# Optimization experiments

Hardware: AMD Instinct MI355X
Metric: run time of the kernel (lower is better)

## Reference

```python
import jax, jax.numpy as jnp
import numpy as np
from jax import lax

D_MODEL = 1024
D_STATE = 16
D_CONV = 4
EXPAND = 2
D_INNER = D_MODEL * EXPAND
EPS = 1e-6


def setup_inputs() -> dict:
    key = jax.random.key(0)
    ks = jax.random.split(key, 8)
    B, L = 2, 1024
    x = jax.random.normal(ks[0], (B, L, D_MODEL), dtype=jnp.float32)
    norm_w = jnp.ones((D_MODEL,), jnp.float32)
    W_in = jax.random.normal(ks[1], (2 * D_INNER, D_MODEL), jnp.float32) * (1.0 / np.sqrt(D_MODEL))
    conv_w = jax.random.normal(ks[2], (D_INNER, 1, D_CONV), jnp.float32) * (1.0 / np.sqrt(D_CONV))
    conv_b = jnp.zeros((D_INNER,), jnp.float32)
    W_x = jax.random.normal(ks[3], (2 * D_STATE + 1, D_INNER), jnp.float32) * (1.0 / np.sqrt(D_INNER))
    A_log = jnp.log(jnp.broadcast_to(jnp.arange(1, D_STATE + 1, dtype=jnp.float32), (D_INNER, D_STATE)))
    D_skip = jnp.ones((D_INNER,), jnp.float32)
    W_dt = jax.random.normal(ks[4], (D_INNER, 1), jnp.float32)
    b_dt = jax.random.normal(ks[5], (D_INNER,), jnp.float32) * 0.1
    W_out = jax.random.normal(ks[6], (D_MODEL, D_INNER), jnp.float32) * (1.0 / np.sqrt(D_INNER))
    return {"x": x, "norm_w": norm_w, "W_in": W_in, "conv_w": conv_w, "conv_b": conv_b,
            "W_x": W_x, "A_log": A_log, "D_skip": D_skip, "W_dt": W_dt, "b_dt": b_dt, "W_out": W_out}


def _selective_scan(x, delta, A, Bp, Cp, D_skip):
    # x, delta: (B, L, D); A: (D, N); Bp, Cp: (B, L, N)
    Bb, L, Dd = x.shape
    N = A.shape[1]

    def step(h, t_in):
        delta_t, B_t, C_t, x_t = t_in           # (B,D),(B,N),(B,N),(B,D)
        dA = jnp.exp(delta_t[..., None] * A)    # (B,D,N)
        h = dA * h + (delta_t * x_t)[..., None] * B_t[:, None, :]
        y_t = jnp.einsum('bdn,bn->bd', h, C_t)
        return h, y_t

    xs = (jnp.moveaxis(delta, 1, 0), jnp.moveaxis(Bp, 1, 0),
          jnp.moveaxis(Cp, 1, 0), jnp.moveaxis(x, 1, 0))
    h0 = jnp.zeros((Bb, Dd, N), x.dtype)
    _, ys = lax.scan(step, h0, xs)              # ys: (L,B,D)
    return jnp.moveaxis(ys, 0, 1) + x * D_skip


def reference(x, norm_w, W_in, conv_w, conv_b, W_x, A_log, D_skip, W_dt, b_dt, W_out):
    residual = x
    # RMSNorm
    xn = x * lax.rsqrt(jnp.mean(x * x, axis=-1, keepdims=True) + EPS) * norm_w
    # in_proj and split
    xz = xn @ W_in.T                              # (B,L,2*Din)
    x_ssm, z = jnp.split(xz, 2, axis=-1)
    # causal depthwise conv1d
    xc = jnp.swapaxes(x_ssm, 1, 2)                # (B,Din,L)
    xc = lax.conv_general_dilated(xc, conv_w, window_strides=(1,),
                                  padding=[(D_CONV - 1, 0)],
                                  feature_group_count=D_INNER,
                                  dimension_numbers=('NCH', 'OIH', 'NCH'))
    xc = xc + conv_b[None, :, None]
    x_ssm = jax.nn.silu(jnp.swapaxes(xc, 1, 2))   # (B,L,Din)
    # input-dependent SSM params
    ssm_params = x_ssm @ W_x.T                    # (B,L,2N+1)
    B_param = ssm_params[:, :, :D_STATE]
    C_param = ssm_params[:, :, D_STATE:2 * D_STATE]
    dt_raw = ssm_params[:, :, -1:]                # (B,L,1)
    delta = jax.nn.softplus(dt_raw * W_dt[:, 0] + b_dt)  # (B,L,Din)
    A = -jnp.exp(A_log)
    y = _selective_scan(x_ssm, delta, A, B_param, C_param, D_skip)
    y = y * jax.nn.silu(z)
    y = y @ W_out.T
    return y + residual
```

## Files before the change

### kernel.cpp

```cpp
#include <hip/hip_runtime.h>
#include <math.h>

#define D_MODEL 1024
#define D_STATE 16
#define D_CONV  4
#define D_INNER 2048
#define LSEQ    1024
#define BATCH   2
#define NROWS   (BATCH * LSEQ)
#define EPSV    1e-6f

#define CHUNK   16
#define NCHUNK  (LSEQ / CHUNK)
#define SSTATE  (BATCH * D_INNER * D_STATE)
#define SROW    36

typedef __attribute__((ext_vector_type(8))) short bf16x8;
typedef __attribute__((ext_vector_type(4))) float f32x4;

__device__ __forceinline__ float silu_f(float x) { return x / (1.0f + __expf(-x)); }
__device__ __forceinline__ float softplus_f(float x) {
    return (x > 20.0f) ? x : __logf(1.0f + __expf(x));
}
__device__ __forceinline__ unsigned short f2bf(float f) {
    unsigned int u = __float_as_uint(f);
    unsigned int r = (u + 0x7FFFu + ((u >> 16) & 1u)) >> 16;
    return (unsigned short)r;
}

__device__ __forceinline__ void pow16(float e1, float* p) {
    float e2 = e1 * e1, e4 = e2 * e2, e8 = e4 * e4;
    p[0] = e1;       p[1] = e2;       p[2] = e2 * e1;  p[3] = e4;
    p[4] = e4 * e1;  p[5] = e4 * e2;  p[6] = e4 * p[2]; p[7] = e8;
    p[8] = e8 * e1;  p[9] = e8 * e2;  p[10] = e8 * p[2]; p[11] = e8 * e4;
    p[12] = e8 * p[4]; p[13] = e8 * p[5]; p[14] = e8 * p[6]; p[15] = e8 * e8;
}

#define WIN_F4   (2 * D_INNER * D_MODEL / 4)
#define WOUT_F4  (D_MODEL * D_INNER / 4)
#define CVT_BLKS ((WIN_F4 + WOUT_F4) / 256)
__global__ __launch_bounds__(256) void prep_kernel(const float* __restrict__ x,
                                                   const float* __restrict__ w,
                                                   unsigned short* __restrict__ xnb,
                                                   const float* __restrict__ w_in,
                                                   unsigned short* __restrict__ w_in_b,
                                                   const float* __restrict__ w_out,
                                                   unsigned short* __restrict__ w_out_b) {
    int blk = blockIdx.x;
    if (blk < NROWS) {
        int row = blk;
        const float4* xr = (const float4*)(x + (size_t)row * D_MODEL);
        float4 v = xr[threadIdx.x];
        float s = v.x * v.x + v.y * v.y + v.z * v.z + v.w * v.w;
#pragma unroll
        for (int off = 32; off > 0; off >>= 1) s += __shfl_down(s, off, 64);
        __shared__ float wsum[4];
        int lane = threadIdx.x & 63, wv = threadIdx.x >> 6;
        if (lane == 0) wsum[wv] = s;
        __syncthreads();
        float tot = wsum[0] + wsum[1] + wsum[2] + wsum[3];
        float scale = rsqrtf(tot * (1.0f / D_MODEL) + EPSV);
        float4 wv4 = ((const float4*)w)[threadIdx.x];
        ushort4 o;
        o.x = f2bf(v.x * scale * wv4.x);
        o.y = f2bf(v.y * scale * wv4.y);
        o.z = f2bf(v.z * scale * wv4.z);
        o.w = f2bf(v.w * scale * wv4.w);
        ((ushort4*)(xnb + (size_t)row * D_MODEL))[threadIdx.x] = o;
    } else {
        int i = (blk - NROWS) * 256 + threadIdx.x;
        const float* src;
        unsigned short* dst;
        int j;
        if (i < WIN_F4) { src = w_in;  dst = w_in_b;  j = i; }
        else            { src = w_out; dst = w_out_b; j = i - WIN_F4; }
        float4 v = ((const float4*)src)[j];
        ushort4 o;
        o.x = f2bf(v.x); o.y = f2bf(v.y); o.z = f2bf(v.z); o.w = f2bf(v.w);
        ((ushort4*)dst)[j] = o;
    }
}

template<int TM, int TN, int BK, int JL>
__global__ __launch_bounds__(256) void gemm_bt_db(const short* __restrict__ A,
                                                  const short* __restrict__ B,
                                                  float* __restrict__ C,
                                                  const float* __restrict__ resid,
                                                  int M, int N, int Klen, int ld) {
    constexpr int MI = TM / 32, NJ = TN / 32;
    constexpr int KC8 = BK / 8;
    __shared__ alignas(16) short As[2][TM * BK];
    __shared__ alignas(16) short Bs[2][TN * BK];
    int tid = threadIdx.x;
    int wave = tid >> 6, lane = tid & 63;
    int wm = (wave >> 1) * (TM / 2), wn = (wave & 1) * (TN / 2);
    int m0 = blockIdx.y * TM, n0 = blockIdx.x * TN;
    int koff = blockIdx.z * Klen;
    C += (size_t)blockIdx.z * M * N;

    f32x4 acc[MI][NJ];
#pragma unroll
    for (int i = 0; i < MI; i++)
#pragma unroll
        for (int j = 0; j < NJ; j++) acc[i][j] = (f32x4){0.f, 0.f, 0.f, 0.f};

    const short* Ab = A + (size_t)m0 * ld + koff;
    const short* Bb = B + (size_t)n0 * ld + koff;
    int qk = (lane >> 4) * 8;
    int rr = lane & 15;

    auto stage = [&](int k0, int buf) {
#pragma unroll
        for (int c0 = 0; c0 < TM * KC8; c0 += 256) {
            int c = c0 + tid;
            __builtin_amdgcn_global_load_lds(
                (const __attribute__((address_space(1))) void*)(Ab + (size_t)(c / KC8) * ld + k0 + (c % KC8) * 8),
                (__attribute__((address_space(3))) void*)(&As[buf][c * 8]), 16, 0, 0);
        }
#pragma unroll
        for (int c0 = 0; c0 < TN * KC8; c0 += 256) {
            int c = c0 + tid;
            __builtin_amdgcn_global_load_lds(
                (const __attribute__((address_space(1))) void*)(Bb + (size_t)(c / KC8) * ld + k0 + (c % KC8) * 8),
                (__attribute__((address_space(3))) void*)(&Bs[buf][c * 8]), 16, 0, 0);
        }
    };

    stage(0, 0);
    int KI = Klen / BK;
    for (int ki = 0; ki < KI; ki++) {
        int b = ki & 1;
        if (ki + 1 < KI) {
            stage((ki + 1) * BK, b ^ 1);
            __builtin_amdgcn_s_waitcnt(0xF70 | JL);
        } else {
            __builtin_amdgcn_s_waitcnt(0xF70);
        }
        __builtin_amdgcn_s_barrier();

#pragma unroll
        for (int kk = 0; kk < BK / 32; kk++) {
            bf16x8 af[MI], bfr[NJ];
#pragma unroll
            for (int i = 0; i < MI; i++)
                af[i] = *(const bf16x8*)(&As[b][(wm + i * 16 + rr) * BK + kk * 32 + qk]);
#pragma unroll
            for (int j = 0; j < NJ; j++)
                bfr[j] = *(const bf16x8*)(&Bs[b][(wn + j * 16 + rr) * BK + kk * 32 + qk]);
#pragma unroll
            for (int i = 0; i < MI; i++)
#pragma unroll
                for (int j = 0; j < NJ; j++)
                    acc[i][j] = __builtin_amdgcn_mfma_f32_16x16x32_bf16(af[i], bfr[j], acc[i][j], 0, 0, 0);
        }
        __builtin_amdgcn_s_barrier();
    }

    int q4 = (lane >> 4) * 4;
#pragma unroll
    for (int i = 0; i < MI; i++) {
#pragma unroll
        for (int j = 0; j < NJ; j++) {
            int n = n0 + wn + j * 16 + rr;
#pragma unroll
            for (int v = 0; v < 4; v++) {
                int mm = m0 + wm + i * 16 + q4 + v;
                float val = acc[i][j][v];
                if (resid) val += resid[(size_t)mm * N + n];
                C[(size_t)mm * N + n] = val;
            }
        }
    }
}

#define PR 4
__global__ __launch_bounds__(256) void params_kernel(const float* __restrict__ xz,
                                                     const float* __restrict__ w,
                                                     const float* __restrict__ cb,
                                                     const float* __restrict__ Wx,
                                                     float* __restrict__ ssm) {
    int r0 = blockIdx.x * PR;
    int bb = r0 >> 10, l0 = r0 & (LSEQ - 1);
    __shared__ alignas(16) float xs[PR][D_INNER];
    const float* xbase = xz + (size_t)(bb * LSEQ) * (2 * D_INNER);
    const float4* W4 = (const float4*)w;

    for (int half = 0; half < 2; half++) {
        int c4 = threadIdx.x + half * 256;
        int d = c4 * 4;
        float4 wA = W4[d + 0], wB = W4[d + 1], wC = W4[d + 2], wD = W4[d + 3];
        float4 bias = ((const float4*)cb)[c4];
        float4 win[PR + 3];
#pragma unroll
        for (int k = 0; k < PR + 3; k++) {
            int l = l0 + k - 3;
            if (l >= 0)
                win[k] = ((const float4*)(xbase + (size_t)l * (2 * D_INNER)))[c4];
            else
                win[k] = (float4){0.f, 0.f, 0.f, 0.f};
        }
#pragma unroll
        for (int j = 0; j < PR; j++) {
            float4 o;
            o.x = bias.x + wA.x * win[j].x + wA.y * win[j + 1].x + wA.z * win[j + 2].x + wA.w * win[j + 3].x;
            o.y = bias.y + wB.x * win[j].y + wB.y * win[j + 1].y + wB.z * win[j + 2].y + wB.w * win[j + 3].y;
            o.z = bias.z + wC.x * win[j].z + wC.y * win[j + 1].z + wC.z * win[j + 2].z + wC.w * win[j + 3].z;
            o.w = bias.w + wD.x * win[j].w + wD.y * win[j + 1].w + wD.z * win[j + 2].w + wD.w * win[j + 3].w;
            o.x = silu_f(o.x); o.y = silu_f(o.y); o.z = silu_f(o.z); o.w = silu_f(o.w);
            *(float4*)&xs[j][c4 * 4] = o;
        }
    }
    __syncthreads();

    int lane = threadIdx.x & 63, wv = threadIdx.x >> 6;
    for (int n = wv; n < 2 * D_STATE + 1; n += 4) {
        const float4* wrow = (const float4*)(Wx + (size_t)n * D_INNER);
        float s0 = 0.f, s1 = 0.f, s2 = 0.f, s3 = 0.f;
#pragma unroll
        for (int c = 0; c < D_INNER / 4 / 64; c++) {
            int k = c * 64 + lane;
            float4 wk = wrow[k];
            float4 a0 = *(const float4*)&xs[0][k * 4];
            float4 a1 = *(const float4*)&xs[1][k * 4];
            float4 a2 = *(const float4*)&xs[2][k * 4];
            float4 a3 = *(const float4*)&xs[3][k * 4];
            s0 += a0.x * wk.x + a0.y * wk.y + a0.z * wk.z + a0.w * wk.w;
            s1 += a1.x * wk.x + a1.y * wk.y + a1.z * wk.z + a1.w * wk.w;
            s2 += a2.x * wk.x + a2.y * wk.y + a2.z * wk.z + a2.w * wk.w;
            s3 += a3.x * wk.x + a3.y * wk.y + a3.z * wk.z + a3.w * wk.w;
        }
#pragma unroll
        for (int off = 32; off > 0; off >>= 1) {
            s0 += __shfl_down(s0, off, 64);
            s1 += __shfl_down(s1, off, 64);
            s2 += __shfl_down(s2, off, 64);
            s3 += __shfl_down(s3, off, 64);
        }
        if (lane == 0) {
            ssm[(size_t)(r0 + 0) * 33 + n] = s0;
            ssm[(size_t)(r0 + 1) * 33 + n] = s1;
            ssm[(size_t)(r0 + 2) * 33 + n] = s2;
            ssm[(size_t)(r0 + 3) * 33 + n] = s3;
        }
    }
}

__device__ __forceinline__ void stage_ssm(const float* __restrict__ ssm,
                                          float* __restrict__ s_ssm,
                                          int bb, int c, int tid) {
    int t = tid >> 4, j = tid & 15;
    const float* g = ssm + (size_t)(bb * LSEQ + c * CHUNK + t) * 33;
    float* s = s_ssm + t * SROW;
    for (int col = j; col < 33; col += 16) s[col] = g[col];
}

__device__ __forceinline__ void stage_tile(const float* __restrict__ g,
                                           float (*dst)[256], int rs, int tid) {
#pragma unroll
    for (int i = 0; i < CHUNK / 4; i++) {
        int f = i * 256 + tid;
        int t = f >> 6;
        int c4 = f & 63;
        ((float4*)&dst[t][0])[c4] = ((const float4*)g)[(size_t)t * rs + c4];
    }
}

__device__ __forceinline__ void stage_halo(const float* __restrict__ gx,
                                           float (*xh)[256], int l0, int tid) {
    if (tid < 192) {
        int t = tid >> 6, c4 = tid & 63;
        float4 v = (float4){0.f, 0.f, 0.f, 0.f};
        if (l0 - 3 + t >= 0)
            v = ((const float4*)(gx - (3 - t) * (2 * D_INNER)))[c4];
        *(float4*)&xh[t][c4 * 4] = v;
    }
}

__global__ __launch_bounds__(256, 4) void scanA_kernel(const float* __restrict__ ssm,
                                                       const float* __restrict__ xz,
                                                       const float* __restrict__ convw,
                                                       const float* __restrict__ cbias,
                                                       const float* __restrict__ Wdt,
                                                       const float* __restrict__ bdt,
                                                       float* __restrict__ P,
                                                       float* __restrict__ Q) {
    int c = blockIdx.x, dg = blockIdx.y, bb = blockIdx.z;
    int tid = threadIdx.x;
    int d = dg * 256 + tid;
    __shared__ alignas(16) float s_ssm[CHUNK * SROW];
    __shared__ alignas(16) float xh[3][256];
    __shared__ alignas(16) float xs[CHUNK][256];
    int l0 = c * CHUNK;
    const float* gx = xz + ((size_t)(bb * LSEQ + l0)) * (2 * D_INNER) + dg * 256;
    stage_ssm(ssm, s_ssm, bb, c, tid);
    stage_tile(gx, xs, 2 * D_INNER / 4, tid);
    stage_halo(gx, xh, l0, tid);
    __syncthreads();

    float4 cw = ((const float4*)convw)[d];
    float cbv = cbias[d];
    float wdt = Wdt[d], bdtv = bdt[d];
    float xm3 = xh[0][tid], xm2 = xh[1][tid], xm1 = xh[2][tid];

    float h[16];
#pragma unroll
    for (int n = 0; n < 16; n++) h[n] = 0.f;
    float sd = 0.f;

#pragma unroll 2
    for (int t = 0; t < CHUNK; t++) {
        float x0 = xs[t][tid];
        float cv = cbv + cw.x * xm3 + cw.y * xm2 + cw.z * xm1 + cw.w * x0;
        float xt = silu_f(cv);
        xm3 = xm2; xm2 = xm1; xm1 = x0;
        float dtr = s_ssm[t * SROW + 32];
        float dlt = softplus_f(dtr * wdt + bdtv);
        float u = dlt * xt;
        sd += dlt;
        float e1 = __expf(-dlt);
        float pw[16];
        pow16(e1, pw);
        const float4* Bq = (const float4*)&s_ssm[t * SROW];
#pragma unroll
        for (int r = 0; r < 4; r++) {
            float4 Bv = Bq[r];
            h[r * 4 + 0] = pw[r * 4 + 0] * h[r * 4 + 0] + u * Bv.x;
            h[r * 4 + 1] = pw[r * 4 + 1] * h[r * 4 + 1] + u * Bv.y;
            h[r * 4 + 2] = pw[r * 4 + 2] * h[r * 4 + 2] + u * Bv.z;
            h[r * 4 + 3] = pw[r * 4 + 3] * h[r * 4 + 3] + u * Bv.w;
        }
    }
    size_t idx = (size_t)c * SSTATE + ((size_t)bb * D_INNER + d) * 16;
    float E = __expf(-sd);
    float pw[16];
    pow16(E, pw);
#pragma unroll
    for (int r = 0; r < 4; r++) {
        float4 pv, qv;
        pv.x = pw[r * 4 + 0]; pv.y = pw[r * 4 + 1];
        pv.z = pw[r * 4 + 2]; pv.w = pw[r * 4 + 3];
        qv.x = h[r * 4 + 0]; qv.y = h[r * 4 + 1];
        qv.z = h[r * 4 + 2]; qv.w = h[r * 4 + 3];
        *(float4*)(P + idx + r * 4) = pv;
        *(float4*)(Q + idx + r * 4) = qv;
    }
}

__global__ __launch_bounds__(256) void scanB_kernel(float* __restrict__ P,
                                                    const float* __restrict__ Q) {
    int bdn = blockIdx.x * 256 + threadIdx.x;
    float H = 0.0f;
#pragma unroll 8
    for (int c = 0; c < NCHUNK; c++) {
        size_t idx = (size_t)c * SSTATE + bdn;
        float p = P[idx], q = Q[idx];
        P[idx] = H;
        H = p * H + q;
    }
}

__global__ __launch_bounds__(256, 4) void scanC_kernel(const float* __restrict__ ssm,
                                                       const float* __restrict__ xz,
                                                       const float* __restrict__ convw,
                                                       const float* __restrict__ cbias,
                                                       const float* __restrict__ Wdt,
                                                       const float* __restrict__ bdt,
                                                       const float* __restrict__ Hs,
                                                       const float* __restrict__ Dskip,
                                                       unsigned short* __restrict__ yb) {
    int c = blockIdx.x, dg = blockIdx.y, bb = blockIdx.z;
    int tid = threadIdx.x;
    int d = dg * 256 + tid;
    __shared__ alignas(16) float s_ssm[CHUNK * SROW];
    __shared__ alignas(16) float xh[3][256];
    __shared__ alignas(16) float xs[CHUNK][256];
    __shared__ alignas(16) float zs[CHUNK][256];
    int l0 = c * CHUNK;
    const float* gx = xz + ((size_t)(bb * LSEQ + l0)) * (2 * D_INNER) + dg * 256;
    stage_ssm(ssm, s_ssm, bb, c, tid);
    stage_tile(gx, xs, 2 * D_INNER / 4, tid);
    stage_halo(gx, xh, l0, tid);
    stage_tile(gx + D_INNER, zs, 2 * D_INNER / 4, tid);
    __syncthreads();

    float4 cw = ((const float4*)convw)[d];
    float cbv = cbias[d];
    float wdt = Wdt[d], bdtv = bdt[d], dsk = Dskip[d];
    float xm3 = xh[0][tid], xm2 = xh[1][tid], xm1 = xh[2][tid];

    float h[16];
    {
        size_t idx = (size_t)c * SSTATE + ((size_t)bb * D_INNER + d) * 16;
#pragma unroll
        for (int r = 0; r < 4; r++) {
            float4 hv = *(const float4*)(Hs + idx + r * 4);
            h[r * 4 + 0] = hv.x; h[r * 4 + 1] = hv.y;
            h[r * 4 + 2] = hv.z; h[r * 4 + 3] = hv.w;
        }
    }
    unsigned short* yg = yb + ((size_t)(bb * LSEQ + c * CHUNK)) * D_INNER + d;

#pragma unroll 2
    for (int t = 0; t < CHUNK; t++) {
        float x0 = xs[t][tid];
        float cv = cbv + cw.x * xm3 + cw.y * xm2 + cw.z * xm1 + cw.w * x0;
        float xt = silu_f(cv);
        xm3 = xm2; xm2 = xm1; xm1 = x0;
        float dtr = s_ssm[t * SROW + 32];
        float dlt = softplus_f(dtr * wdt + bdtv);
        float zt = zs[t][tid];
        float u = dlt * xt;
        float e1 = __expf(-dlt);
        float pw[16];
        pow16(e1, pw);
        const float4* Bq = (const float4*)&s_ssm[t * SROW];
        const float4* Cq = (const float4*)&s_ssm[t * SROW + 16];
        float y = 0.f;
#pragma unroll
        for (int r = 0; r < 4; r++) {
            float4 Bv = Bq[r];
            float4 Cv = Cq[r];
            h[r * 4 + 0] = pw[r * 4 + 0] * h[r * 4 + 0] + u * Bv.x;
            h[r * 4 + 1] = pw[r * 4 + 1] * h[r * 4 + 1] + u * Bv.y;
            h[r * 4 + 2] = pw[r * 4 + 2] * h[r * 4 + 2] + u * Bv.z;
            h[r * 4 + 3] = pw[r * 4 + 3] * h[r * 4 + 3] + u * Bv.w;
            y += h[r * 4 + 0] * Cv.x + h[r * 4 + 1] * Cv.y
               + h[r * 4 + 2] * Cv.z + h[r * 4 + 3] * Cv.w;
        }
        float o = (y + xt * dsk) * silu_f(zt);
        yg[(size_t)t * D_INNER] = f2bf(o);
    }
}

extern "C" void kernel_launch(void* const* d_in, const int* in_sizes, int n_in,
                              void* d_out, int out_size, void* d_ws, size_t ws_size,
                              hipStream_t stream) {
    const float* x      = (const float*)d_in[0];
    const float* norm_w = (const float*)d_in[1];
    const float* W_in   = (const float*)d_in[2];
    const float* conv_w = (const float*)d_in[3];
    const float* conv_b = (const float*)d_in[4];
    const float* W_x    = (const float*)d_in[5];
    const float* D_skip = (const float*)d_in[7];
    const float* W_dt   = (const float*)d_in[8];
    const float* b_dt   = (const float*)d_in[9];
    const float* W_out  = (const float*)d_in[10];
    float* out = (float*)d_out;

    float* ws = (float*)d_ws;
    float* xz    = ws;
    float* Pbuf  = xz + (size_t)NROWS * 2 * D_INNER;
    float* ssm   = Pbuf + (size_t)NCHUNK * SSTATE;
    float* after = ssm + (size_t)NROWS * 33;
    unsigned short* xnb    = (unsigned short*)after;
    unsigned short* W_in_b = (unsigned short*)(after + 1024 * 1024);
    unsigned short* W_out_b= (unsigned short*)(after + 3 * 1024 * 1024);
    unsigned short* ybuf_b = (unsigned short*)(after + 4 * 1024 * 1024);
    float* Qbuf  = after + 4 * 1024 * 1024;

    prep_kernel<<<NROWS + CVT_BLKS, 256, 0, stream>>>(x, norm_w, xnb,
                                                      W_in, W_in_b, W_out, W_out_b);
    {
        dim3 grid(2 * D_INNER / 128, NROWS / 128, 1);
        gemm_bt_db<128, 128, 32, 4><<<grid, 256, 0, stream>>>(
            (const short*)xnb, (const short*)W_in_b, xz, nullptr,
            NROWS, 2 * D_INNER, D_MODEL, D_MODEL);
    }
    params_kernel<<<NROWS / PR, 256, 0, stream>>>(xz, conv_w, conv_b, W_x, ssm);
    {
        dim3 grid(NCHUNK, D_INNER / 256, BATCH);
        scanA_kernel<<<grid, 256, 0, stream>>>(ssm, xz, conv_w, conv_b,
                                               W_dt, b_dt, Pbuf, Qbuf);
        scanB_kernel<<<SSTATE / 256, 256, 0, stream>>>(Pbuf, Qbuf);
        scanC_kernel<<<grid, 256, 0, stream>>>(ssm, xz, conv_w, conv_b,
                                               W_dt, b_dt, Pbuf, D_skip, ybuf_b);
    }
    {
        dim3 grid(D_MODEL / 64, NROWS / 64, 1);
        gemm_bt_db<64, 64, 64, 4><<<grid, 256, 0, stream>>>(
            (const short*)ybuf_b, (const short*)W_out_b, out, x,
            NROWS, D_MODEL, D_INNER, D_INNER);
    }
}
```

Before: 218.9 us.

## Fuse chunk-state scan into scanA via last-block atomic counter, double chunk size

New measurement: 322.3 us. 1.47x slower.

```diff
diff --git a/kernel.cpp b/kernel.cpp
--- a/kernel.cpp
+++ b/kernel.cpp
@@ -10,7 +10,7 @@
 #define NROWS   (BATCH * LSEQ)
 #define EPSV    1e-6f
 
-#define CHUNK   16
+#define CHUNK   32
 #define NCHUNK  (LSEQ / CHUNK)
 #define SSTATE  (BATCH * D_INNER * D_STATE)
 #define SROW    36
@@ -178,7 +178,9 @@
                                                      const float* __restrict__ w,
                                                      const float* __restrict__ cb,
                                                      const float* __restrict__ Wx,
-                                                     float* __restrict__ ssm) {
+                                                     float* __restrict__ ssm,
+                                                     unsigned int* __restrict__ cnt) {
+    if (blockIdx.x == 0 && threadIdx.x < 16) cnt[threadIdx.x] = 0u;
     int r0 = blockIdx.x * PR;
     int bb = r0 >> 10, l0 = r0 & (LSEQ - 1);
     __shared__ alignas(16) float xs[PR][D_INNER];
@@ -248,10 +250,10 @@
 __device__ __forceinline__ void stage_ssm(const float* __restrict__ ssm,
                                           float* __restrict__ s_ssm,
                                           int bb, int c, int tid) {
-    int t = tid >> 4, j = tid & 15;
+    int t = tid >> 3, j = tid & 7;
     const float* g = ssm + (size_t)(bb * LSEQ + c * CHUNK + t) * 33;
     float* s = s_ssm + t * SROW;
-    for (int col = j; col < 33; col += 16) s[col] = g[col];
+    for (int col = j; col < 33; col += 8) s[col] = g[col];
 }
 
 __device__ __forceinline__ void stage_tile(const float* __restrict__ g,
@@ -276,14 +278,15 @@
     }
 }
 
-__global__ __launch_bounds__(256, 4) void scanA_kernel(const float* __restrict__ ssm,
-                                                       const float* __restrict__ xz,
-                                                       const float* __restrict__ convw,
-                                                       const float* __restrict__ cbias,
-                                                       const float* __restrict__ Wdt,
-                                                       const float* __restrict__ bdt,
-                                                       float* __restrict__ P,
-                                                       float* __restrict__ Q) {
+__global__ __launch_bounds__(256) void scanA_kernel(const float* __restrict__ ssm,
+                                                    const float* __restrict__ xz,
+                                                    const float* __restrict__ convw,
+                                                    const float* __restrict__ cbias,
+                                                    const float* __restrict__ Wdt,
+                                                    const float* __restrict__ bdt,
+                                                    float* __restrict__ P,
+                                                    float* __restrict__ Q,
+                                                    unsigned int* __restrict__ cnt) {
     int c = blockIdx.x, dg = blockIdx.y, bb = blockIdx.z;
     int tid = threadIdx.x;
     int d = dg * 256 + tid;
@@ -344,30 +347,42 @@
         *(float4*)(P + idx + r * 4) = pv;
         *(float4*)(Q + idx + r * 4) = qv;
     }
-}
-
-__global__ __launch_bounds__(256) void scanB_kernel(float* __restrict__ P,
-                                                    const float* __restrict__ Q) {
-    int bdn = blockIdx.x * 256 + threadIdx.x;
-    float H = 0.0f;
-#pragma unroll 8
-    for (int c = 0; c < NCHUNK; c++) {
-        size_t idx = (size_t)c * SSTATE + bdn;
-        float p = P[idx], q = Q[idx];
-        P[idx] = H;
-        H = p * H + q;
-    }
-}
-
-__global__ __launch_bounds__(256, 4) void scanC_kernel(const float* __restrict__ ssm,
-                                                       const float* __restrict__ xz,
-                                                       const float* __restrict__ convw,
-                                                       const float* __restrict__ cbias,
-                                                       const float* __restrict__ Wdt,
-                                                       const float* __restrict__ bdt,
-                                                       const float* __restrict__ Hs,
-                                                       const float* __restrict__ Dskip,
-                                                       unsigned short* __restrict__ yb) {
+
+    __threadfence();
+    __shared__ int is_last;
+    if (tid == 0) {
+        unsigned t = atomicAdd(&cnt[bb * 8 + dg], 1u);
+        is_last = (t == NCHUNK - 1);
+    }
+    __syncthreads();
+    if (is_last) {
+        __threadfence();
+        size_t colbase = ((size_t)bb * D_INNER + dg * 256) * 16;
+        float H[16];
+#pragma unroll
+        for (int k = 0; k < 16; k++) H[k] = 0.f;
+        for (int cc = 0; cc < NCHUNK; cc++) {
+            size_t base = (size_t)cc * SSTATE + colbase;
+#pragma unroll
+            for (int k = 0; k < 16; k++) {
+                size_t ix = base + (size_t)k * 256 + tid;
+                float p = P[ix], q = Q[ix];
+                P[ix] = H[k];
+                H[k] = p * H[k] + q;
+            }
+        }
+    }
+}
+
+__global__ __launch_bounds__(256) void scanC_kernel(const float* __restrict__ ssm,
+                                                    const float* __restrict__ xz,
+                                                    const float* __restrict__ convw,
+                                                    const float* __restrict__ cbias,
+                                                    const float* __restrict__ Wdt,
+                                                    const float* __restrict__ bdt,
+                                                    const float* __restrict__ Hs,
+                                                    const float* __restrict__ Dskip,
+                                                    unsigned short* __restrict__ yb) {
     int c = blockIdx.x, dg = blockIdx.y, bb = blockIdx.z;
     int tid = threadIdx.x;
     int d = dg * 256 + tid;
@@ -448,14 +463,16 @@
     float* out = (float*)d_out;
 
     float* ws = (float*)d_ws;
-    float* xz    = ws;
-    float* Pbuf  = xz + (size_t)NROWS * 2 * D_INNER;
-    float* ssm   = Pbuf + (size_t)NCHUNK * SSTATE;
-    float* after = ssm + (size_t)NROWS * 33;
+    float* xz      = ws;
+    float* xconv   = xz + (size_t)NROWS * 2 * D_INNER;
+    unsigned int* cnt = (unsigned int*)xconv;
+    float* ssm     = xconv + (size_t)NROWS * D_INNER;
+    float* after   = ssm + (size_t)NROWS * 33;
     unsigned short* xnb    = (unsigned short*)after;
     unsigned short* W_in_b = (unsigned short*)(after + 1024 * 1024);
     unsigned short* W_out_b= (unsigned short*)(after + 3 * 1024 * 1024);
     unsigned short* ybuf_b = (unsigned short*)(after + 4 * 1024 * 1024);
+    float* Pbuf  = after;
     float* Qbuf  = after + 4 * 1024 * 1024;
 
     prep_kernel<<<NROWS + CVT_BLKS, 256, 0, stream>>>(x, norm_w, xnb,
@@ -466,18 +483,17 @@
             (const short*)xnb, (const short*)W_in_b, xz, nullptr,
             NROWS, 2 * D_INNER, D_MODEL, D_MODEL);
     }
-    params_kernel<<<NROWS / PR, 256, 0, stream>>>(xz, conv_w, conv_b, W_x, ssm);
+    params_kernel<<<NROWS / PR, 256, 0, stream>>>(xz, conv_w, conv_b, W_x, ssm, cnt);
     {
         dim3 grid(NCHUNK, D_INNER / 256, BATCH);
         scanA_kernel<<<grid, 256, 0, stream>>>(ssm, xz, conv_w, conv_b,
-                                               W_dt, b_dt, Pbuf, Qbuf);
-        scanB_kernel<<<SSTATE / 256, 256, 0, stream>>>(Pbuf, Qbuf);
+                                               W_dt, b_dt, Pbuf, Qbuf, cnt);
         scanC_kernel<<<grid, 256, 0, stream>>>(ssm, xz, conv_w, conv_b,
                                                W_dt, b_dt, Pbuf, D_skip, ybuf_b);
     }
     {
         dim3 grid(D_MODEL / 64, NROWS / 64, 1);
-        gemm_bt_db<64, 64, 64, 4><<<grid, 256, 0, stream>>>(
+        gemm_bt_db<64, 64, 32, 2><<<grid, 256, 0, stream>>>(
             (const short*)ybuf_b, (const short*)W_out_b, out, x,
             NROWS, D_MODEL, D_INNER, D_INNER);
     }
```

## Compute local chunk outputs in scanA and apply closed-form carry correction in scanC

Applied to the files above, without the earlier changes.

Result: no change. 220.4 us (+0.7%).

```diff
diff --git a/kernel.cpp b/kernel.cpp
--- a/kernel.cpp
+++ b/kernel.cpp
@@ -10,7 +10,7 @@
 #define NROWS   (BATCH * LSEQ)
 #define EPSV    1e-6f
 
-#define CHUNK   16
+#define CHUNK   32
 #define NCHUNK  (LSEQ / CHUNK)
 #define SSTATE  (BATCH * D_INNER * D_STATE)
 #define SROW    36
@@ -248,10 +248,10 @@
 __device__ __forceinline__ void stage_ssm(const float* __restrict__ ssm,
                                           float* __restrict__ s_ssm,
                                           int bb, int c, int tid) {
-    int t = tid >> 4, j = tid & 15;
+    int t = tid >> 3, j = tid & 7;
     const float* g = ssm + (size_t)(bb * LSEQ + c * CHUNK + t) * 33;
     float* s = s_ssm + t * SROW;
-    for (int col = j; col < 33; col += 16) s[col] = g[col];
+    for (int col = j; col < 33; col += 8) s[col] = g[col];
 }
 
 __device__ __forceinline__ void stage_tile(const float* __restrict__ g,
@@ -276,14 +276,17 @@
     }
 }
 
-__global__ __launch_bounds__(256, 4) void scanA_kernel(const float* __restrict__ ssm,
-                                                       const float* __restrict__ xz,
-                                                       const float* __restrict__ convw,
-                                                       const float* __restrict__ cbias,
-                                                       const float* __restrict__ Wdt,
-                                                       const float* __restrict__ bdt,
-                                                       float* __restrict__ P,
-                                                       float* __restrict__ Q) {
+__global__ __launch_bounds__(256) void scanA_kernel(const float* __restrict__ ssm,
+                                                    const float* __restrict__ xz,
+                                                    const float* __restrict__ convw,
+                                                    const float* __restrict__ cbias,
+                                                    const float* __restrict__ Wdt,
+                                                    const float* __restrict__ bdt,
+                                                    const float* __restrict__ Dskip,
+                                                    float* __restrict__ P,
+                                                    float* __restrict__ Q,
+                                                    float* __restrict__ Sbuf,
+                                                    float* __restrict__ ydbuf) {
     int c = blockIdx.x, dg = blockIdx.y, bb = blockIdx.z;
     int tid = threadIdx.x;
     int d = dg * 256 + tid;
@@ -299,8 +302,11 @@
 
     float4 cw = ((const float4*)convw)[d];
     float cbv = cbias[d];
-    float wdt = Wdt[d], bdtv = bdt[d];
+    float wdt = Wdt[d], bdtv = bdt[d], dsk = Dskip[d];
     float xm3 = xh[0][tid], xm2 = xh[1][tid], xm1 = xh[2][tid];
+
+    float* Sg = Sbuf + (size_t)(bb * LSEQ + l0) * D_INNER + d;
+    float* Yg = ydbuf + (size_t)(bb * LSEQ + l0) * D_INNER + d;
 
     float h[16];
 #pragma unroll
@@ -321,99 +327,6 @@
         float pw[16];
         pow16(e1, pw);
         const float4* Bq = (const float4*)&s_ssm[t * SROW];
-#pragma unroll
-        for (int r = 0; r < 4; r++) {
-            float4 Bv = Bq[r];
-            h[r * 4 + 0] = pw[r * 4 + 0] * h[r * 4 + 0] + u * Bv.x;
-            h[r * 4 + 1] = pw[r * 4 + 1] * h[r * 4 + 1] + u * Bv.y;
-            h[r * 4 + 2] = pw[r * 4 + 2] * h[r * 4 + 2] + u * Bv.z;
-            h[r * 4 + 3] = pw[r * 4 + 3] * h[r * 4 + 3] + u * Bv.w;
-        }
-    }
-    size_t idx = (size_t)c * SSTATE + ((size_t)bb * D_INNER + d) * 16;
-    float E = __expf(-sd);
-    float pw[16];
-    pow16(E, pw);
-#pragma unroll
-    for (int r = 0; r < 4; r++) {
-        float4 pv, qv;
-        pv.x = pw[r * 4 + 0]; pv.y = pw[r * 4 + 1];
-        pv.z = pw[r * 4 + 2]; pv.w = pw[r * 4 + 3];
-        qv.x = h[r * 4 + 0]; qv.y = h[r * 4 + 1];
-        qv.z = h[r * 4 + 2]; qv.w = h[r * 4 + 3];
-        *(float4*)(P + idx + r * 4) = pv;
-        *(float4*)(Q + idx + r * 4) = qv;
-    }
-}
-
-__global__ __launch_bounds__(256) void scanB_kernel(float* __restrict__ P,
-                                                    const float* __restrict__ Q) {
-    int bdn = blockIdx.x * 256 + threadIdx.x;
-    float H = 0.0f;
-#pragma unroll 8
-    for (int c = 0; c < NCHUNK; c++) {
-        size_t idx = (size_t)c * SSTATE + bdn;
-        float p = P[idx], q = Q[idx];
-        P[idx] = H;
-        H = p * H + q;
-    }
-}
-
-__global__ __launch_bounds__(256, 4) void scanC_kernel(const float* __restrict__ ssm,
-                                                       const float* __restrict__ xz,
-                                                       const float* __restrict__ convw,
-                                                       const float* __restrict__ cbias,
-                                                       const float* __restrict__ Wdt,
-                                                       const float* __restrict__ bdt,
-                                                       const float* __restrict__ Hs,
-                                                       const float* __restrict__ Dskip,
-                                                       unsigned short* __restrict__ yb) {
-    int c = blockIdx.x, dg = blockIdx.y, bb = blockIdx.z;
-    int tid = threadIdx.x;
-    int d = dg * 256 + tid;
-    __shared__ alignas(16) float s_ssm[CHUNK * SROW];
-    __shared__ alignas(16) float xh[3][256];
-    __shared__ alignas(16) float xs[CHUNK][256];
-    __shared__ alignas(16) float zs[CHUNK][256];
-    int l0 = c * CHUNK;
-    const float* gx = xz + ((size_t)(bb * LSEQ + l0)) * (2 * D_INNER) + dg * 256;
-    stage_ssm(ssm, s_ssm, bb, c, tid);
-    stage_tile(gx, xs, 2 * D_INNER / 4, tid);
-    stage_halo(gx, xh, l0, tid);
-    stage_tile(gx + D_INNER, zs, 2 * D_INNER / 4, tid);
-    __syncthreads();
-
-    float4 cw = ((const float4*)convw)[d];
-    float cbv = cbias[d];
-    float wdt = Wdt[d], bdtv = bdt[d], dsk = Dskip[d];
-    float xm3 = xh[0][tid], xm2 = xh[1][tid], xm1 = xh[2][tid];
-
-    float h[16];
-    {
-        size_t idx = (size_t)c * SSTATE + ((size_t)bb * D_INNER + d) * 16;
-#pragma unroll
-        for (int r = 0; r < 4; r++) {
-            float4 hv = *(const float4*)(Hs + idx + r * 4);
-            h[r * 4 + 0] = hv.x; h[r * 4 + 1] = hv.y;
-            h[r * 4 + 2] = hv.z; h[r * 4 + 3] = hv.w;
-        }
-    }
-    unsigned short* yg = yb + ((size_t)(bb * LSEQ + c * CHUNK)) * D_INNER + d;
-
-#pragma unroll 2
-    for (int t = 0; t < CHUNK; t++) {
-        float x0 = xs[t][tid];
-        float cv = cbv + cw.x * xm3 + cw.y * xm2 + cw.z * xm1 + cw.w * x0;
-        float xt = silu_f(cv);
-        xm3 = xm2; xm2 = xm1; xm1 = x0;
-        float dtr = s_ssm[t * SROW + 32];
-        float dlt = softplus_f(dtr * wdt + bdtv);
-        float zt = zs[t][tid];
-        float u = dlt * xt;
-        float e1 = __expf(-dlt);
-        float pw[16];
-        pow16(e1, pw);
-        const float4* Bq = (const float4*)&s_ssm[t * SROW];
         const float4* Cq = (const float4*)&s_ssm[t * SROW + 16];
         float y = 0.f;
 #pragma unroll
@@ -427,7 +340,95 @@
             y += h[r * 4 + 0] * Cv.x + h[r * 4 + 1] * Cv.y
                + h[r * 4 + 2] * Cv.z + h[r * 4 + 3] * Cv.w;
         }
-        float o = (y + xt * dsk) * silu_f(zt);
+        Sg[(size_t)t * D_INNER] = sd;
+        Yg[(size_t)t * D_INNER] = y + xt * dsk;
+    }
+    size_t idx = (size_t)c * SSTATE + ((size_t)bb * D_INNER + d) * 16;
+    float E = __expf(-sd);
+    float pw[16];
+    pow16(E, pw);
+#pragma unroll
+    for (int r = 0; r < 4; r++) {
+        float4 pv, qv;
+        pv.x = pw[r * 4 + 0]; pv.y = pw[r * 4 + 1];
+        pv.z = pw[r * 4 + 2]; pv.w = pw[r * 4 + 3];
+        qv.x = h[r * 4 + 0]; qv.y = h[r * 4 + 1];
+        qv.z = h[r * 4 + 2]; qv.w = h[r * 4 + 3];
+        *(float4*)(P + idx + r * 4) = pv;
+        *(float4*)(Q + idx + r * 4) = qv;
+    }
+}
+
+__global__ __launch_bounds__(256) void scanB_kernel(float* __restrict__ P,
+                                                    const float* __restrict__ Q) {
+    int bdn = blockIdx.x * 256 + threadIdx.x;
+    float p[NCHUNK], q[NCHUNK], hs[NCHUNK];
+#pragma unroll
+    for (int c = 0; c < NCHUNK; c++) {
+        size_t ix = (size_t)c * SSTATE + bdn;
+        p[c] = P[ix];
+        q[c] = Q[ix];
+    }
+    float H = 0.0f;
+#pragma unroll
+    for (int c = 0; c < NCHUNK; c++) {
+        hs[c] = H;
+        H = p[c] * H + q[c];
+    }
+#pragma unroll
+    for (int c = 0; c < NCHUNK; c++)
+        P[(size_t)c * SSTATE + bdn] = hs[c];
+}
+
+__global__ __launch_bounds__(256) void scanC_kernel(const float* __restrict__ ssm,
+                                                    const float* __restrict__ xz,
+                                                    const float* __restrict__ Sbuf,
+                                                    const float* __restrict__ ydbuf,
+                                                    const float* __restrict__ Hs,
+                                                    unsigned short* __restrict__ yb) {
+    int c = blockIdx.x, dg = blockIdx.y, bb = blockIdx.z;
+    int tid = threadIdx.x;
+    int d = dg * 256 + tid;
+    __shared__ alignas(16) float s_ssm[CHUNK * SROW];
+    stage_ssm(ssm, s_ssm, bb, c, tid);
+
+    float H0[16];
+    {
+        size_t idx = (size_t)c * SSTATE + ((size_t)bb * D_INNER + d) * 16;
+#pragma unroll
+        for (int r = 0; r < 4; r++) {
+            float4 hv = *(const float4*)(Hs + idx + r * 4);
+            H0[r * 4 + 0] = hv.x; H0[r * 4 + 1] = hv.y;
+            H0[r * 4 + 2] = hv.z; H0[r * 4 + 3] = hv.w;
+        }
+    }
+    __syncthreads();
+
+    size_t r0g = (size_t)(bb * LSEQ + c * CHUNK);
+    const float* Sg = Sbuf + r0g * D_INNER + d;
+    const float* Yg = ydbuf + r0g * D_INNER + d;
+    const float* Zg = xz + r0g * (2 * D_INNER) + D_INNER + d;
+    unsigned short* yg = yb + r0g * D_INNER + d;
+
+#pragma unroll 4
+    for (int t = 0; t < CHUNK; t++) {
+        float S  = Sg[(size_t)t * D_INNER];
+        float yd = Yg[(size_t)t * D_INNER];
+        float zt = Zg[(size_t)t * 2 * D_INNER];
+        float E = __expf(-S);
+        float pw[16];
+        pow16(E, pw);
+        const float4* Cq = (const float4*)&s_ssm[t * SROW + 16];
+        float corr = 0.f;
+#pragma unroll
+        for (int r = 0; r < 4; r++) {
+            float4 Cv = Cq[r];
+            corr += (Cv.x * pw[r * 4 + 0]) * H0[r * 4 + 0]
+                  + (Cv.y * pw[r * 4 + 1]) * H0[r * 4 + 1]
+                  + (Cv.z * pw[r * 4 + 2]) * H0[r * 4 + 2]
+                  + (Cv.w * pw[r * 4 + 3]) * H0[r * 4 + 3];
+        }
+        float o = (yd + corr) * silu_f(zt);
         yg[(size_t)t * D_INNER] = f2bf(o);
     }
 }
@@ -449,14 +450,16 @@
 
     float* ws = (float*)d_ws;
     float* xz    = ws;
-    float* Pbuf  = xz + (size_t)NROWS * 2 * D_INNER;
-    float* ssm   = Pbuf + (size_t)NCHUNK * SSTATE;
+    float* Sbuf  = xz + (size_t)NROWS * 2 * D_INNER;
+    float* ssm   = Sbuf + (size_t)NROWS * D_INNER;
     float* after = ssm + (size_t)NROWS * 33;
     unsigned short* xnb    = (unsigned short*)after;
     unsigned short* W_in_b = (unsigned short*)(after + 1024 * 1024);
     unsigned short* W_out_b= (unsigned short*)(after + 3 * 1024 * 1024);
     unsigned short* ybuf_b = (unsigned short*)(after + 4 * 1024 * 1024);
+    float* Pbuf  = after;
     float* Qbuf  = after + 4 * 1024 * 1024;
+    float* ydbuf = after + 8 * 1024 * 1024;
 
     prep_kernel<<<NROWS + CVT_BLKS, 256, 0, stream>>>(x, norm_w, xnb,
                                                       W_in, W_in_b, W_out, W_out_b);
@@ -470,14 +473,15 @@
     {
         dim3 grid(NCHUNK, D_INNER / 256, BATCH);
         scanA_kernel<<<grid, 256, 0, stream>>>(ssm, xz, conv_w, conv_b,
-                                               W_dt, b_dt, Pbuf, Qbuf);
+                                               W_dt, b_dt, D_skip,
+                                               Pbuf, Qbuf, Sbuf, ydbuf);
         scanB_kernel<<<SSTATE / 256, 256, 0, stream>>>(Pbuf, Qbuf);
-        scanC_kernel<<<grid, 256, 0, stream>>>(ssm, xz, conv_w, conv_b,
-                                               W_dt, b_dt, Pbuf, D_skip, ybuf_b);
+        scanC_kernel<<<grid, 256, 0, stream>>>(ssm, xz, Sbuf, ydbuf,
+                                               Pbuf, ybuf_b);
     }
     {
         dim3 grid(D_MODEL / 64, NROWS / 64, 1);
-        gemm_bt_db<64, 64, 64, 4><<<grid, 256, 0, stream>>>(
+        gemm_bt_db<64, 64, 32, 2><<<grid, 256, 0, stream>>>(
             (const short*)ybuf_b, (const short*)W_out_b, out, x,
             NROWS, D_MODEL, D_INNER, D_INNER);
     }
```
